# Kernel tuning notes

Hardware: AMD Instinct MI355X
Metric: run time of the kernel (lower is better)

The kernel has to match this reference:

```python
import jax, jax.numpy as jnp
import numpy as np

D_EMB = 1024
D_HEAD = 64
B = 4
T = 4096


def setup_inputs() -> dict:
    key = jax.random.key(0)
    kx, kk, kq, kv = jax.random.split(key, 4)
    s = 1.0 / np.sqrt(D_EMB)  # torch Linear default init scale (uniform bound)
    x = jax.random.normal(kx, (B, T, D_EMB), dtype=jnp.float32)
    Wk = jax.random.uniform(kk, (D_HEAD, D_EMB), jnp.float32, -s, s)
    Wq = jax.random.uniform(kq, (D_HEAD, D_EMB), jnp.float32, -s, s)
    Wv = jax.random.uniform(kv, (D_HEAD, D_EMB), jnp.float32, -s, s)
    return {"x": x, "Wk": Wk, "Wq": Wq, "Wv": Wv}


def reference(x, Wk, Wq, Wv):
    # x: (B, T, d_emb); W*: (d_head, d_emb) -- torch Linear stores (out, in)
    k = jnp.einsum('bte,he->bth', x, Wk)
    q = jnp.einsum('bte,he->bth', x, Wq)
    v = jnp.einsum('bte,he->bth', x, Wv)
    scale = D_HEAD ** (-0.5)
    a = jnp.einsum('bth,bsh->bts', q, k) * scale  # (B, T, T)
    Tlen = x.shape[-2]
    causal = jnp.tril(jnp.ones((Tlen, Tlen), dtype=bool))
    a = jnp.where(causal, a, -jnp.inf)
    a = jax.nn.softmax(a, axis=-1)
    return jnp.einsum('bts,bsh->bth', a, v)  # (B, T, d_head)
```

## Files before the change

kernel.cpp:

```cpp
#include <hip/hip_runtime.h>
#include <hip/hip_bf16.h>

#define D_EMB 1024
#define T_LEN 4096
#define NTASK2 544

typedef short short8 __attribute__((ext_vector_type(8)));
typedef float f32x4 __attribute__((ext_vector_type(4)));
typedef float f32x16 __attribute__((ext_vector_type(16)));
typedef float float4v __attribute__((ext_vector_type(4)));

__device__ __forceinline__ unsigned short f32_to_bf16(float f) {
    union { float f; unsigned int u; } c; c.f = f;
    unsigned int u = c.u;
    return (unsigned short)((u + 0x7FFFu + ((u >> 16) & 1u)) >> 16);
}
__device__ __forceinline__ float bf16_to_f32(unsigned short v) {
    union { unsigned int u; float f; } c; c.u = ((unsigned int)v) << 16;
    return c.f;
}
__device__ __forceinline__ unsigned cvtpk_bf16(float a, float b) {
    unsigned r;
    asm("v_cvt_pk_bf16_f32 %0, %1, %2" : "=v"(r) : "v"(a), "v"(b));
    return r;
}
__device__ __forceinline__ float xhalf_max(float x) {
    return fmaxf(x, __shfl_xor(x, 32));
}
__device__ __forceinline__ float xhalf_add(float x) {
    return x + __shfl_xor(x, 32);
}
__device__ __forceinline__ void gl_lds16(const void* g, void* l) {
    __builtin_amdgcn_global_load_lds(
        (const __attribute__((address_space(1))) unsigned int*)(g),
        (__attribute__((address_space(3))) unsigned int*)(l), 16, 0, 0);
}

#define QSCALE (0.125f * 1.44269504f)

__global__ __launch_bounds__(256) void convert_w(const float* __restrict__ Wk,
                                                 const float* __restrict__ Wq,
                                                 const float* __restrict__ Wv,
                                                 unsigned short* __restrict__ Wb) {
    int e = (blockIdx.x * 256 + threadIdx.x) * 8;
    const float* src;
    if (e < 65536) src = Wk + e;
    else if (e < 131072) src = Wq + (e - 65536);
    else src = Wv + (e - 131072);
    float4v a0 = *(const float4v*)src;
    float4v a1 = *(const float4v*)(src + 4);
    short8 r;
    r[0] = (short)f32_to_bf16(a0[0]); r[1] = (short)f32_to_bf16(a0[1]);
    r[2] = (short)f32_to_bf16(a0[2]); r[3] = (short)f32_to_bf16(a0[3]);
    r[4] = (short)f32_to_bf16(a1[0]); r[5] = (short)f32_to_bf16(a1[1]);
    r[6] = (short)f32_to_bf16(a1[2]); r[7] = (short)f32_to_bf16(a1[3]);
    int row = e >> 10;
    int dst = e ^ ((row & 7) << 3);
    *(short8*)(Wb + dst) = r;
}

__global__ __launch_bounds__(256, 2) void qkv_proj(const float* __restrict__ x,
                                                   const unsigned short* __restrict__ Wb,
                                                   unsigned short* __restrict__ Kb,
                                                   unsigned short* __restrict__ Qb,
                                                   unsigned short* __restrict__ Vt) {
    __shared__ __attribute__((aligned(16))) unsigned short Wsl[2][12288];

    int tid = threadIdx.x;
    int lane = tid & 63, wave = tid >> 6;
    int lo = lane & 15, hi = lane >> 4;
    int rg = wave >> 1, nh = wave & 1;
    int row0 = blockIdx.x * 32;

    const float* xp = x + (size_t)(row0 + rg * 16 + lo) * D_EMB + hi * 8;

    f32x4 acc[6];
#pragma unroll
    for (int i = 0; i < 6; i++) acc[i] = (f32x4){0.f, 0.f, 0.f, 0.f};

    float4v xa0 = *(const float4v*)(xp);
    float4v xa1 = *(const float4v*)(xp + 4);
    float4v xa2 = *(const float4v*)(xp + 32);
    float4v xa3 = *(const float4v*)(xp + 36);
#pragma unroll
    for (int j = 0; j < 6; j++) {
        int unit = j * 4 + wave;
        int u = unit * 64 + lane;
        gl_lds16(Wb + (size_t)(u >> 3) * D_EMB + (u & 7) * 8, &Wsl[0][unit * 512]);
    }

    int buf = 0;
    int xorm = (lo & 7) << 4;
    int rowbase = nh * 96 + lo;

    for (int kt = 0; kt < 16; kt++) {
        float4v xn0, xn1, xn2, xn3;
        if (kt < 15) {
            const float* pn = xp + (kt + 1) * 64;
            xn0 = *(const float4v*)(pn);
            xn1 = *(const float4v*)(pn + 4);
            xn2 = *(const float4v*)(pn + 32);
            xn3 = *(const float4v*)(pn + 36);
            int k0n = (kt + 1) * 64;
#pragma unroll
            for (int j = 0; j < 6; j++) {
                int unit = j * 4 + wave;
                int u = unit * 64 + lane;
                gl_lds16(Wb + (size_t)(u >> 3) * D_EMB + k0n + (u & 7) * 8,
                         &Wsl[buf ^ 1][unit * 512]);
            }
        }
        __builtin_amdgcn_sched_barrier(0);
        if (kt < 15) {
            asm volatile("s_waitcnt vmcnt(8)" ::: "memory");
        } else {
            asm volatile("s_waitcnt vmcnt(0)" ::: "memory");
        }
        __builtin_amdgcn_s_barrier();
        __builtin_amdgcn_sched_barrier(0);

        short8 af[2];
        {
            union { unsigned u[4]; short8 s; } c;
            c.u[0] = cvtpk_bf16(xa0[0], xa0[1]);
            c.u[1] = cvtpk_bf16(xa0[2], xa0[3]);
            c.u[2] = cvtpk_bf16(xa1[0], xa1[1]);
            c.u[3] = cvtpk_bf16(xa1[2], xa1[3]);
            af[0] = c.s;
            c.u[0] = cvtpk_bf16(xa2[0], xa2[1]);
            c.u[1] = cvtpk_bf16(xa2[2], xa2[3]);
            c.u[2] = cvtpk_bf16(xa3[0], xa3[1]);
            c.u[3] = cvtpk_bf16(xa3[2], xa3[3]);
            af[1] = c.s;
        }
        const char* sb = (const char*)&Wsl[buf][0];
#pragma unroll
        for (int i = 0; i < 6; i++) {
            int row = rowbase + i * 16;
#pragma unroll
            for (int ks = 0; ks < 2; ks++) {
                short8 bfrag = *(const short8*)(sb + row * 128 + ((ks * 64 + hi * 16) ^ xorm));
                acc[i] = __builtin_amdgcn_mfma_f32_16x16x32_bf16(af[ks], bfrag, acc[i], 0, 0, 0);
            }
        }
        buf ^= 1;
        if (kt < 15) { xa0 = xn0; xa1 = xn1; xa2 = xn2; xa3 = xn3; }
    }

#pragma unroll
    for (int i = 0; i < 6; i++) {
        int n = nh * 6 + i;
#pragma unroll
        for (int r = 0; r < 4; r++) {
            int grow = row0 + rg * 16 + hi * 4 + r;
            float val = acc[i][r];
            if (n < 4) {
                Kb[(size_t)grow * 64 + n * 16 + lo] = f32_to_bf16(val);
            } else if (n < 8) {
                Qb[(size_t)grow * 64 + (n - 4) * 16 + lo] = f32_to_bf16(val * QSCALE);
            } else {
                int bb = grow >> 12;
                Vt[((size_t)bb * 64 + (n - 8) * 16 + lo) * T_LEN + (grow & 4095)] = f32_to_bf16(val);
            }
        }
    }
}

__global__ __launch_bounds__(64, 3) void attn(const unsigned short* __restrict__ Qb,
                                              const unsigned short* __restrict__ Kb,
                                              const unsigned short* __restrict__ Vt,
                                              unsigned short* __restrict__ Opart,
                                              float* __restrict__ Mpart,
                                              float* __restrict__ Lpart) {
    int lane = threadIdx.x;
    int q32 = lane & 31;
    int hi = lane >> 5;
    unsigned lin = blockIdx.x;
    int b = lin & 3;
    int s = (int)(((lin >> 3) << 1) | ((lin >> 2) & 1));

    int k = 16, rem = s;
    while (rem >= 4 * k) { rem -= 4 * k; k--; }
    int ti = rem / k;
    int st = 4 * k - 1 - ti;
    int c = rem - ti * k;

    int u0 = c * 8;
    int u1 = min(u0 + 8, 2 * st + 2);
    int ta = 2 * st, tb = ta + 1;
    int qrowA = 64 * st + q32;
    int qrowB = qrowA + 32;

    size_t base = (size_t)b * T_LEN;

    short8 qfa[4], qfb[4];
    const unsigned short* qpa = Qb + (base + qrowA) * 64 + hi * 8;
    const unsigned short* qpb = Qb + (base + qrowB) * 64 + hi * 8;
#pragma unroll
    for (int d = 0; d < 4; d++) {
        qfa[d] = *(const short8*)(qpa + d * 16);
        qfb[d] = *(const short8*)(qpb + d * 16);
    }

    size_t vbase = ((size_t)b * 64 + q32) * T_LEN;
    f32x16 oA0 = {0.f}, oA1 = {0.f}, oB0 = {0.f}, oB1 = {0.f};
    float mA = -3e38f, lA = 0.f, mB = -3e38f, lB = 0.f;

    for (int u = u0; u < u1; ++u) {
        const unsigned short* kp = Kb + (base + u * 32 + q32) * 64 + hi * 8;
        short8 kc0 = *(const short8*)kp;
        short8 kc1 = *(const short8*)(kp + 16);
        short8 kc2 = *(const short8*)(kp + 32);
        short8 kc3 = *(const short8*)(kp + 48);
        const unsigned short* vp = Vt + vbase + u * 32 + hi * 8;
        short8 vc0 = *(const short8*)vp;
        short8 vc1 = *(const short8*)(vp + 16);
        short8 vc2 = *(const short8*)(vp + 32 * T_LEN);
        short8 vc3 = *(const short8*)(vp + 32 * T_LEN + 16);

        f32x16 sa = {0.f}, sb = {0.f};
        sa = __builtin_amdgcn_mfma_f32_32x32x16_bf16(kc0, qfa[0], sa, 0, 0, 0);
        sb = __builtin_amdgcn_mfma_f32_32x32x16_bf16(kc0, qfb[0], sb, 0, 0, 0);
        sa = __builtin_amdgcn_mfma_f32_32x32x16_bf16(kc1, qfa[1], sa, 0, 0, 0);
        sb = __builtin_amdgcn_mfma_f32_32x32x16_bf16(kc1, qfb[1], sb, 0, 0, 0);
        sa = __builtin_amdgcn_mfma_f32_32x32x16_bf16(kc2, qfa[2], sa, 0, 0, 0);
        sb = __builtin_amdgcn_mfma_f32_32x32x16_bf16(kc2, qfb[2], sb, 0, 0, 0);
        sa = __builtin_amdgcn_mfma_f32_32x32x16_bf16(kc3, qfa[3], sa, 0, 0, 0);
        sb = __builtin_amdgcn_mfma_f32_32x32x16_bf16(kc3, qfb[3], sb, 0, 0, 0);

        if (u >= ta) {
#pragma unroll
            for (int r = 0; r < 16; ++r) {
                int key = 32 * u + (r & 3) + 8 * (r >> 2) + 4 * hi;
                sa[r] = (key <= qrowA) ? sa[r] : -3e38f;
                if (u == tb) sb[r] = (key <= qrowB) ? sb[r] : -3e38f;
            }
        }

        float a0 = fmaxf(fmaxf(sa[0], sa[1]), sa[2]);
        float a1 = fmaxf(fmaxf(sa[3], sa[4]), sa[5]);
        float a2 = fmaxf(fmaxf(sa[6], sa[7]), sa[8]);
        float a3 = fmaxf(fmaxf(sa[9], sa[10]), sa[11]);
        float a4 = fmaxf(fmaxf(sa[12], sa[13]), sa[14]);
        float mxA = fmaxf(fmaxf(fmaxf(a0, a1), fmaxf(a2, a3)), fmaxf(a4, sa[15]));
        float b0 = fmaxf(fmaxf(sb[0], sb[1]), sb[2]);
        float b1 = fmaxf(fmaxf(sb[3], sb[4]), sb[5]);
        float b2 = fmaxf(fmaxf(sb[6], sb[7]), sb[8]);
        float b3 = fmaxf(fmaxf(sb[9], sb[10]), sb[11]);
        float b4 = fmaxf(fmaxf(sb[12], sb[13]), sb[14]);
        float mxB = fmaxf(fmaxf(fmaxf(b0, b1), fmaxf(b2, b3)), fmaxf(b4, sb[15]));
        mxA = xhalf_max(mxA);
        mxB = xhalf_max(mxB);

        float grow = fmaxf(mxA - mA, mxB - mB);
        if (__any(grow > 8.0f)) {
            float mnA = fmaxf(mA, mxA);
            float alA = exp2f(mA - mnA);
            mA = mnA; lA *= alA;
            float mnB = fmaxf(mB, mxB);
            float alB = exp2f(mB - mnB);
            mB = mnB; lB *= alB;
#pragma unroll
            for (int r = 0; r < 16; ++r) {
                oA0[r] *= alA; oA1[r] *= alA;
                oB0[r] *= alB; oB1[r] *= alB;
            }
        }

#pragma unroll
        for (int r = 0; r < 16; ++r) {
            sa[r] = exp2f(sa[r] - mA);
            sb[r] = exp2f(sb[r] - mB);
        }
        float yA = ((sa[0] + sa[8]) + (sa[4] + sa[12])) + ((sa[1] + sa[9]) + (sa[5] + sa[13]))
                 + ((sa[2] + sa[10]) + (sa[6] + sa[14])) + ((sa[3] + sa[11]) + (sa[7] + sa[15]));
        float yB = ((sb[0] + sb[8]) + (sb[4] + sb[12])) + ((sb[1] + sb[9]) + (sb[5] + sb[13]))
                 + ((sb[2] + sb[10]) + (sb[6] + sb[14])) + ((sb[3] + sb[11]) + (sb[7] + sb[15]));
        lA += xhalf_add(yA);
        lB += xhalf_add(yB);

        unsigned pa0 = cvtpk_bf16(sa[0],  sa[1]);
        unsigned pa1 = cvtpk_bf16(sa[2],  sa[3]);
        unsigned pa2 = cvtpk_bf16(sa[4],  sa[5]);
        unsigned pa3 = cvtpk_bf16(sa[6],  sa[7]);
        unsigned pa4 = cvtpk_bf16(sa[8],  sa[9]);
        unsigned pa5 = cvtpk_bf16(sa[10], sa[11]);
        unsigned pa6 = cvtpk_bf16(sa[12], sa[13]);
        unsigned pa7 = cvtpk_bf16(sa[14], sa[15]);
        unsigned pb0 = cvtpk_bf16(sb[0],  sb[1]);
        unsigned pb1 = cvtpk_bf16(sb[2],  sb[3]);
        unsigned pb2 = cvtpk_bf16(sb[4],  sb[5]);
        unsigned pb3 = cvtpk_bf16(sb[6],  sb[7]);
        unsigned pb4 = cvtpk_bf16(sb[8],  sb[9]);
        unsigned pb5 = cvtpk_bf16(sb[10], sb[11]);
        unsigned pb6 = cvtpk_bf16(sb[12], sb[13]);
        unsigned pb7 = cvtpk_bf16(sb[14], sb[15]);
        asm("v_permlane32_swap_b32 %0, %1" : "+v"(pa0), "+v"(pa2));
        asm("v_permlane32_swap_b32 %0, %1" : "+v"(pa1), "+v"(pa3));
        asm("v_permlane32_swap_b32 %0, %1" : "+v"(pa4), "+v"(pa6));
        asm("v_permlane32_swap_b32 %0, %1" : "+v"(pa5), "+v"(pa7));
        asm("v_permlane32_swap_b32 %0, %1" : "+v"(pb0), "+v"(pb2));
        asm("v_permlane32_swap_b32 %0, %1" : "+v"(pb1), "+v"(pb3));
        asm("v_permlane32_swap_b32 %0, %1" : "+v"(pb4), "+v"(pb6));
        asm("v_permlane32_swap_b32 %0, %1" : "+v"(pb5), "+v"(pb7));
        union U8 { unsigned u[4]; short8 s; };
        U8 fA0; fA0.u[0] = pa0; fA0.u[1] = pa1; fA0.u[2] = pa2; fA0.u[3] = pa3;
        U8 fA1; fA1.u[0] = pa4; fA1.u[1] = pa5; fA1.u[2] = pa6; fA1.u[3] = pa7;
        U8 fB0; fB0.u[0] = pb0; fB0.u[1] = pb1; fB0.u[2] = pb2; fB0.u[3] = pb3;
        U8 fB1; fB1.u[0] = pb4; fB1.u[1] = pb5; fB1.u[2] = pb6; fB1.u[3] = pb7;

        oA0 = __builtin_amdgcn_mfma_f32_32x32x16_bf16(vc0, fA0.s, oA0, 0, 0, 0);
        oB0 = __builtin_amdgcn_mfma_f32_32x32x16_bf16(vc0, fB0.s, oB0, 0, 0, 0);
        oA0 = __builtin_amdgcn_mfma_f32_32x32x16_bf16(vc1, fA1.s, oA0, 0, 0, 0);
        oB0 = __builtin_amdgcn_mfma_f32_32x32x16_bf16(vc1, fB1.s, oB0, 0, 0, 0);
        oA1 = __builtin_amdgcn_mfma_f32_32x32x16_bf16(vc2, fA0.s, oA1, 0, 0, 0);
        oB1 = __builtin_amdgcn_mfma_f32_32x32x16_bf16(vc2, fB0.s, oB1, 0, 0, 0);
        oA1 = __builtin_amdgcn_mfma_f32_32x32x16_bf16(vc3, fA1.s, oA1, 0, 0, 0);
        oB1 = __builtin_amdgcn_mfma_f32_32x32x16_bf16(vc3, fB1.s, oB1, 0, 0, 0);
    }

    int slotA = (b * NTASK2 + s) * 2;
    size_t tbA = ((size_t)slotA * 32 + q32) * 64;
    size_t tbB = ((size_t)(slotA + 1) * 32 + q32) * 64;
#pragma unroll
    for (int hb = 0; hb < 2; hb++) {
#pragma unroll
        for (int g = 0; g < 4; g++) {
            float eA0 = hb ? oA1[4 * g] : oA0[4 * g];
            float eA1 = hb ? oA1[4 * g + 1] : oA0[4 * g + 1];
            float eA2 = hb ? oA1[4 * g + 2] : oA0[4 * g + 2];
            float eA3 = hb ? oA1[4 * g + 3] : oA0[4 * g + 3];
            float eB0 = hb ? oB1[4 * g] : oB0[4 * g];
            float eB1 = hb ? oB1[4 * g + 1] : oB0[4 * g + 1];
            float eB2 = hb ? oB1[4 * g + 2] : oB0[4 * g + 2];
            float eB3 = hb ? oB1[4 * g + 3] : oB0[4 * g + 3];
            int h0 = hb * 32 + g * 8 + hi * 4;
            *reinterpret_cast<uint2*>(Opart + tbA + h0) =
                make_uint2(cvtpk_bf16(eA0, eA1), cvtpk_bf16(eA2, eA3));
            *reinterpret_cast<uint2*>(Opart + tbB + h0) =
                make_uint2(cvtpk_bf16(eB0, eB1), cvtpk_bf16(eB2, eB3));
        }
    }
    if (lane < 32) {
        Mpart[slotA * 32 + q32] = mA;
        Lpart[slotA * 32 + q32] = lA;
        Mpart[(slotA + 1) * 32 + q32] = mB;
        Lpart[(slotA + 1) * 32 + q32] = lB;
    }
}

__global__ __launch_bounds__(256) void attn_merge(const unsigned short* __restrict__ Opart,
                                                  const float* __restrict__ Mpart,
                                                  const float* __restrict__ Lpart,
                                                  float* __restrict__ out) {
    int tid = threadIdx.x;
    int g = blockIdx.x * 64 + (tid >> 2);
    int h0 = (tid & 3) * 16;
    int b = g >> 12, t = g & 4095;
    int tile32 = t >> 5, r32 = t & 31;
    int st = tile32 >> 1, member = tile32 & 1;
    int k = (st >> 2) + 1;
    int sbase = 4 * (136 - ((k * (k + 1)) >> 1));
    int ti = 4 * k - 1 - st;
    int s0 = sbase + ti * k;
    int slot0 = (b * NTASK2 + s0) * 2 + member;

    float mm = -3e38f;
    for (int i = 0; i < k; i++) mm = fmaxf(mm, Mpart[(slot0 + 2 * i) * 32 + r32]);
    float ll = 0.f;
    float acc[16];
#pragma unroll
    for (int e = 0; e < 16; e++) acc[e] = 0.f;
    for (int i = 0; i < k; i++) {
        int slot = slot0 + 2 * i;
        float a = exp2f(Mpart[slot * 32 + r32] - mm);
        ll += a * Lpart[slot * 32 + r32];
        const unsigned short* op = Opart + ((size_t)slot * 32 + r32) * 64 + h0;
        short8 v0 = *(const short8*)op;
        short8 v1 = *(const short8*)(op + 8);
#pragma unroll
        for (int e = 0; e < 8; e++) {
            acc[e]     += a * bf16_to_f32((unsigned short)v0[e]);
            acc[8 + e] += a * bf16_to_f32((unsigned short)v1[e]);
        }
    }
    float inv = 1.f / ll;
    float* dst = out + (size_t)g * 64 + h0;
#pragma unroll
    for (int e = 0; e < 16; e++) dst[e] = acc[e] * inv;
}

extern "C" void kernel_launch(void* const* d_in, const int* in_sizes, int n_in,
                              void* d_out, int out_size, void* d_ws, size_t ws_size,
                              hipStream_t stream) {
    (void)in_sizes; (void)n_in; (void)out_size; (void)ws_size;
    const float* x  = (const float*)d_in[0];
    const float* Wk = (const float*)d_in[1];
    const float* Wq = (const float*)d_in[2];
    const float* Wv = (const float*)d_in[3];
    float* out = (float*)d_out;

    unsigned short* Wb = (unsigned short*)d_ws;
    unsigned short* Kb = Wb + 196608;
    unsigned short* Qb = Kb + 1048576;
    unsigned short* Vt = Qb + 1048576;
    unsigned short* Opart = Vt + 1048576;
    float* Mpart = (float*)(Opart + (size_t)4 * NTASK2 * 2 * 32 * 64);
    float* Lpart = Mpart + 4 * NTASK2 * 2 * 32;

    hipLaunchKernelGGL(convert_w, dim3(96), dim3(256), 0, stream, Wk, Wq, Wv, Wb);
    hipLaunchKernelGGL(qkv_proj, dim3(512), dim3(256), 0, stream, x, Wb, Kb, Qb, Vt);
    hipLaunchKernelGGL(attn, dim3(4 * NTASK2), dim3(64), 0, stream, Qb, Kb, Vt, Opart, Mpart, Lpart);
    hipLaunchKernelGGL(attn_merge, dim3(256), dim3(256), 0, stream, Opart, Mpart, Lpart, out);
}
```

Before: 79.04 us.

## Stage full x tile in LDS as bf16 and halve rows per QKV block

The QKV projection now processes 16 rows per block instead of 32, launching twice as many blocks. Each block loads its whole 16x1024 x tile up front, converts it to bf16 and stores it swizzled in LDS. Waves then split the 192 output columns (3 MFMA tiles each) instead of splitting rows and column halves. This is meant to raise parallelism and load all of x as one batch rather than a per-step register prefetch. The cost is that W traffic doubles across blocks, LDS use grows, and each k-step gains an extra barrier.

```diff
diff --git a/kernel.cpp b/kernel.cpp
--- a/kernel.cpp
+++ b/kernel.cpp
@@ -64,96 +64,89 @@
                                                    unsigned short* __restrict__ Kb,
                                                    unsigned short* __restrict__ Qb,
                                                    unsigned short* __restrict__ Vt) {
+    __shared__ __attribute__((aligned(16))) unsigned short Xl[16 * 1024];
     __shared__ __attribute__((aligned(16))) unsigned short Wsl[2][12288];
 
     int tid = threadIdx.x;
     int lane = tid & 63, wave = tid >> 6;
     int lo = lane & 15, hi = lane >> 4;
-    int rg = wave >> 1, nh = wave & 1;
-    int row0 = blockIdx.x * 32;
-
-    const float* xp = x + (size_t)(row0 + rg * 16 + lo) * D_EMB + hi * 8;
-
-    f32x4 acc[6];
-#pragma unroll
-    for (int i = 0; i < 6; i++) acc[i] = (f32x4){0.f, 0.f, 0.f, 0.f};
-
-    float4v xa0 = *(const float4v*)(xp);
-    float4v xa1 = *(const float4v*)(xp + 4);
-    float4v xa2 = *(const float4v*)(xp + 32);
-    float4v xa3 = *(const float4v*)(xp + 36);
-#pragma unroll
-    for (int j = 0; j < 6; j++) {
-        int unit = j * 4 + wave;
-        int u = unit * 64 + lane;
-        gl_lds16(Wb + (size_t)(u >> 3) * D_EMB + (u & 7) * 8, &Wsl[0][unit * 512]);
-    }
-
-    int buf = 0;
+    int row0 = blockIdx.x * 16;
+
+    {
+        int r = tid >> 4, ii = tid & 15;
+        const float* xrow = x + (size_t)(row0 + r) * D_EMB + ii * 4;
+        float4v xv[16];
+#pragma unroll
+        for (int j = 0; j < 16; j++) xv[j] = *(const float4v*)(xrow + j * 64);
+#pragma unroll
+        for (int j = 0; j < 6; j++) {
+            int unit = j * 4 + wave;
+            int u = unit * 64 + lane;
+            gl_lds16(Wb + (size_t)(u >> 3) * D_EMB + (u & 7) * 8, &Wsl[0][unit * 512]);
+        }
+        unsigned swz = (unsigned)((r & 7) << 4);
+        char* xl = (char*)Xl + r * 2048;
+#pragma unroll
+        for (int j = 0; j < 16; j++) {
+            unsigned w0 = cvtpk_bf16(xv[j][0], xv[j][1]);
+            unsigned w1 = cvtpk_bf16(xv[j][2], xv[j][3]);
+            *(uint2*)(xl + (((unsigned)(j * 128 + ii * 8)) ^ swz)) = make_uint2(w0, w1);
+        }
+    }
+    __syncthreads();
+
+    f32x4 acc0 = (f32x4){0.f, 0.f, 0.f, 0.f};
+    f32x4 acc1 = (f32x4){0.f, 0.f, 0.f, 0.f};
+    f32x4 acc2 = (f32x4){0.f, 0.f, 0.f, 0.f};
     int xorm = (lo & 7) << 4;
-    int rowbase = nh * 96 + lo;
+    const char* xbase = (const char*)Xl + lo * 2048;
+    int rowb = wave * 48 + lo;
 
     for (int kt = 0; kt < 16; kt++) {
-        float4v xn0, xn1, xn2, xn3;
         if (kt < 15) {
-            const float* pn = xp + (kt + 1) * 64;
-            xn0 = *(const float4v*)(pn);
-            xn1 = *(const float4v*)(pn + 4);
-            xn2 = *(const float4v*)(pn + 32);
-            xn3 = *(const float4v*)(pn + 36);
             int k0n = (kt + 1) * 64;
 #pragma unroll
             for (int j = 0; j < 6; j++) {
                 int unit = j * 4 + wave;
                 int u = unit * 64 + lane;
                 gl_lds16(Wb + (size_t)(u >> 3) * D_EMB + k0n + (u & 7) * 8,
-                         &Wsl[buf ^ 1][unit * 512]);
+                         &Wsl[(kt + 1) & 1][unit * 512]);
             }
-        }
-        __builtin_amdgcn_sched_barrier(0);
-        if (kt < 15) {
-            asm volatile("s_waitcnt vmcnt(8)" ::: "memory");
+            __builtin_amdgcn_sched_barrier(0);
+            asm volatile("s_waitcnt vmcnt(6)" ::: "memory");
         } else {
+            __builtin_amdgcn_sched_barrier(0);
             asm volatile("s_waitcnt vmcnt(0)" ::: "memory");
         }
         __builtin_amdgcn_s_barrier();
         __builtin_amdgcn_sched_barrier(0);
 
-        short8 af[2];
-        {
-            union { unsigned u[4]; short8 s; } c;
-            c.u[0] = cvtpk_bf16(xa0[0], xa0[1]);
-            c.u[1] = cvtpk_bf16(xa0[2], xa0[3]);
-            c.u[2] = cvtpk_bf16(xa1[0], xa1[1]);
-            c.u[3] = cvtpk_bf16(xa1[2], xa1[3]);
-            af[0] = c.s;
-            c.u[0] = cvtpk_bf16(xa2[0], xa2[1]);
-            c.u[1] = cvtpk_bf16(xa2[2], xa2[3]);
-            c.u[2] = cvtpk_bf16(xa3[0], xa3[1]);
-            c.u[3] = cvtpk_bf16(xa3[2], xa3[3]);
-            af[1] = c.s;
-        }
-        const char* sb = (const char*)&Wsl[buf][0];
-#pragma unroll
-        for (int i = 0; i < 6; i++) {
-            int row = rowbase + i * 16;
-#pragma unroll
-            for (int ks = 0; ks < 2; ks++) {
-                short8 bfrag = *(const short8*)(sb + row * 128 + ((ks * 64 + hi * 16) ^ xorm));
-                acc[i] = __builtin_amdgcn_mfma_f32_16x16x32_bf16(af[ks], bfrag, acc[i], 0, 0, 0);
-            }
-        }
-        buf ^= 1;
-        if (kt < 15) { xa0 = xn0; xa1 = xn1; xa2 = xn2; xa3 = xn3; }
-    }
-
-#pragma unroll
-    for (int i = 0; i < 6; i++) {
-        int n = nh * 6 + i;
+        const char* sb = (const char*)&Wsl[kt & 1][0];
+#pragma unroll
+        for (int ks = 0; ks < 2; ks++) {
+            int xoff = (kt * 128 + ks * 64 + hi * 16) ^ xorm;
+            short8 af = *(const short8*)(xbase + xoff);
+            int boff = (ks * 64 + hi * 16) ^ xorm;
+            short8 b0 = *(const short8*)(sb + rowb * 128 + boff);
+            short8 b1 = *(const short8*)(sb + (rowb + 16) * 128 + boff);
+            short8 b2 = *(const short8*)(sb + (rowb + 32) * 128 + boff);
+            acc0 = __builtin_amdgcn_mfma_f32_16x16x32_bf16(af, b0, acc0, 0, 0, 0);
+            acc1 = __builtin_amdgcn_mfma_f32_16x16x32_bf16(af, b1, acc1, 0, 0, 0);
+            acc2 = __builtin_amdgcn_mfma_f32_16x16x32_bf16(af, b2, acc2, 0, 0, 0);
+        }
+        asm volatile("s_waitcnt lgkmcnt(0)" ::: "memory");
+        __builtin_amdgcn_s_barrier();
+        __builtin_amdgcn_sched_barrier(0);
+    }
+
+    f32x4 accs[3] = {acc0, acc1, acc2};
+#pragma unroll
+    for (int i = 0; i < 3; i++) {
+        int n = wave * 3 + i;
 #pragma unroll
         for (int r = 0; r < 4; r++) {
-            int grow = row0 + rg * 16 + hi * 4 + r;
-            float val = acc[i][r];
+            int grow = row0 + hi * 4 + r;
+            float val = accs[i][r];
             if (n < 4) {
                 Kb[(size_t)grow * 64 + n * 16 + lo] = f32_to_bf16(val);
             } else if (n < 8) {
@@ -409,7 +402,7 @@
     float* Lpart = Mpart + 4 * NTASK2 * 2 * 32;
 
     hipLaunchKernelGGL(convert_w, dim3(96), dim3(256), 0, stream, Wk, Wq, Wv, Wb);
-    hipLaunchKernelGGL(qkv_proj, dim3(512), dim3(256), 0, stream, x, Wb, Kb, Qb, Vt);
+    hipLaunchKernelGGL(qkv_proj, dim3(1024), dim3(256), 0, stream, x, Wb, Kb, Qb, Vt);
     hipLaunchKernelGGL(attn, dim3(4 * NTASK2), dim3(64), 0, stream, Qb, Kb, Vt, Opart, Mpart, Lpart);
     hipLaunchKernelGGL(attn_merge, dim3(256), dim3(256), 0, stream, Opart, Mpart, Lpart, out);
 }
```

After: 84.18 us. +6.5%, slower.
